# Kernel tuning notes

Hardware: AMD Instinct MI355X
Metric: run time of the kernel (lower is better)

Reference implementation:

```python
import jax, jax.numpy as jnp
import numpy as np

NUM_HEADS = 16
HIDDEN = 1024
HEAD_DIM = HIDDEN // NUM_HEADS


def setup_inputs() -> dict:
    key = jax.random.key(0)
    ks = jax.random.split(key, 9)
    B, S, D = 2, 2048, HIDDEN
    s = 1.0 / np.sqrt(D)
    return {
        "x": jax.random.normal(ks[0], (B, S, D), dtype=jnp.float32),
        "Wq": jax.random.normal(ks[1], (D, D), dtype=jnp.float32) * s,
        "bq": jnp.zeros((D,), dtype=jnp.float32),
        "Wk": jax.random.normal(ks[2], (D, D), dtype=jnp.float32) * s,
        "bk": jnp.zeros((D,), dtype=jnp.float32),
        "Wv": jax.random.normal(ks[3], (D, D), dtype=jnp.float32) * s,
        "bv": jnp.zeros((D,), dtype=jnp.float32),
        "Wo": jax.random.normal(ks[4], (D, D), dtype=jnp.float32) * s,
        "bo": jnp.zeros((D,), dtype=jnp.float32),
    }


def reference(x, Wq, bq, Wk, bk, Wv, bv, Wo, bo):
    B, S, D = x.shape
    H, Hd = NUM_HEADS, HEAD_DIM
    # projections -> [B, H, S, Hd]
    def proj(W, b):
        return (x @ W + b).reshape(B, S, H, Hd).transpose(0, 2, 1, 3)
    q = proj(Wq, bq)
    k = proj(Wk, bk)
    v = proj(Wv, bv)
    scores = jnp.einsum('bhqd,bhkd->bhqk', q, k) / jnp.sqrt(jnp.float32(Hd))
    p_attn = jax.nn.softmax(scores, axis=-1)  # dropout = identity (eval)
    ctx = jnp.einsum('bhqk,bhkd->bhqd', p_attn, v)
    attn_mean = jnp.mean(p_attn, axis=1)  # [B, S, S]
    out = ctx.transpose(0, 2, 1, 3).reshape(B, S, D) @ Wo + bo
    return out, attn_mean
```

## Files before the change

kernel.cpp:

```cpp
#include <hip/hip_runtime.h>
#include <math.h>

#define NUM_HEADS 16
#define HEAD_DIM  64
#define HIDDEN    1024
#define BATCH     2
#define SEQ       2048

#define QSCALE 0.1803368801111204f

typedef short bf16x8 __attribute__((ext_vector_type(8)));
typedef short short4v __attribute__((ext_vector_type(4)));
typedef float f32x4 __attribute__((ext_vector_type(4)));

#if __has_builtin(__builtin_amdgcn_exp2f)
#define EXP2F __builtin_amdgcn_exp2f
#else
#define EXP2F exp2f
#endif

__device__ __forceinline__ short f2bf(float f) {
    union { float f; unsigned int u; } x; x.f = f;
    unsigned int r = x.u + 0x7fffu + ((x.u >> 16) & 1u);
    return (short)(r >> 16);
}

__device__ __forceinline__ unsigned int pack_bf16_trunc(float lo, float hi) {
    return __builtin_amdgcn_perm(__float_as_uint(hi), __float_as_uint(lo), 0x07060302u);
}

__device__ __forceinline__ void async16(const void* g, void* l) {
    __builtin_amdgcn_global_load_lds(
        (const __attribute__((address_space(1))) void*)g,
        (__attribute__((address_space(3))) void*)l, 16, 0, 0);
}

__global__ __launch_bounds__(256)
void convert_x_kernel(const float* __restrict__ x, short* __restrict__ xb)
{
    size_t i = ((size_t)blockIdx.x * 256 + threadIdx.x) * 4;
    float4 v = *(const float4*)&x[i];
    short4v o;
    o.x = f2bf(v.x); o.y = f2bf(v.y); o.z = f2bf(v.z); o.w = f2bf(v.w);
    *(short4v*)&xb[i] = o;
}

__global__ __launch_bounds__(256)
void transpose_w_kernel(const float* __restrict__ Wq, const float* __restrict__ Wk,
                        const float* __restrict__ Wv, const float* __restrict__ Wo,
                        short* __restrict__ Wt4)
{
    __shared__ float t[64][65];
    const int tid = threadIdx.x;
    const int z = blockIdx.z;
    const float* W = (z == 0) ? Wq : (z == 1) ? Wk : (z == 2) ? Wv : Wo;
    short* dst = Wt4 + (size_t)z * HIDDEN * HIDDEN;
    const int c0 = blockIdx.x * 64;
    const int r0 = blockIdx.y * 64;
    const int cl = tid & 63, rw = tid >> 6;
    #pragma unroll
    for (int p = 0; p < 16; ++p) {
        int row = p * 4 + rw;
        t[row][cl] = W[(size_t)(r0 + row) * HIDDEN + c0 + cl];
    }
    __syncthreads();
    #pragma unroll
    for (int p = 0; p < 16; ++p) {
        int orow = p * 4 + rw;
        dst[(size_t)(c0 + orow) * HIDDEN + r0 + cl] = f2bf(t[cl][orow]);
    }
}

__global__ __launch_bounds__(256)
void qkv_proj_kernel(const short* __restrict__ xb, const short* __restrict__ Wt4,
                     const float* __restrict__ bq, const float* __restrict__ bk,
                     const float* __restrict__ bv,
                     short* __restrict__ Qb, short* __restrict__ Kb,
                     short* __restrict__ Vt)
{
    __shared__ short ldsA[128 * 32];
    __shared__ short ldsB[128 * 32];
    const int tid = threadIdx.x;
    const int lane = tid & 63, w = tid >> 6;
    const int l = lane & 15, q = lane >> 4;
    const int n0 = blockIdx.x * 128;
    const int m0 = blockIdx.y * 128;
    const int z  = blockIdx.z;
    const short* Wt = Wt4 + (size_t)z * HIDDEN * HIDDEN;
    const int wm = (w >> 1) * 64, wn = (w & 1) * 64;
    const int kc = q ^ ((l >> 1) & 3);

    f32x4 acc[4][4];
    #pragma unroll
    for (int i = 0; i < 4; ++i)
        #pragma unroll
        for (int j = 0; j < 4; ++j)
            acc[i][j] = (f32x4){0.f, 0.f, 0.f, 0.f};

    for (int k0 = 0; k0 < HIDDEN; k0 += 32) {
        #pragma unroll
        for (int half = 0; half < 2; ++half) {
            int c = half * 256 + tid;
            int row = c >> 2;
            int kcg = (c & 3) ^ ((row >> 1) & 3);
            async16(xb + (size_t)(m0 + row) * HIDDEN + k0 + kcg * 8, &ldsA[c * 8]);
            async16(Wt + (size_t)(n0 + row) * HIDDEN + k0 + kcg * 8, &ldsB[c * 8]);
        }
        __syncthreads();
        bf16x8 af[4], bfr[4];
        #pragma unroll
        for (int i = 0; i < 4; ++i)
            af[i] = *(const bf16x8*)&ldsA[((wm + 16 * i + l) * 4 + kc) * 8];
        #pragma unroll
        for (int j = 0; j < 4; ++j)
            bfr[j] = *(const bf16x8*)&ldsB[((wn + 16 * j + l) * 4 + kc) * 8];
        #pragma unroll
        for (int i = 0; i < 4; ++i)
            #pragma unroll
            for (int j = 0; j < 4; ++j)
                acc[i][j] = __builtin_amdgcn_mfma_f32_16x16x32_bf16(
                    af[i], bfr[j], acc[i][j], 0, 0, 0);
        __syncthreads();
    }

    const float* bias = (z == 0) ? bq : (z == 1) ? bk : bv;
    const float sc = (z == 0) ? QSCALE : 1.0f;
    if (z < 2) {
        short* Ob = (z == 0) ? Qb : Kb;
        #pragma unroll
        for (int j = 0; j < 4; ++j) {
            int n = n0 + wn + 16 * j + l;
            float bval = bias[n];
            int h = n >> 6, hd = n & 63;
            #pragma unroll
            for (int i = 0; i < 4; ++i) {
                #pragma unroll
                for (int reg = 0; reg < 4; ++reg) {
                    int m = m0 + wm + 16 * i + 4 * q + reg;
                    int b_ = m >> 11, s = m & 2047;
                    Ob[(((size_t)(b_ * NUM_HEADS + h) * SEQ) + s) * HEAD_DIM + hd] =
                        f2bf((acc[i][j][reg] + bval) * sc);
                }
            }
        }
    } else {
        #pragma unroll
        for (int j = 0; j < 4; ++j) {
            int n = n0 + wn + 16 * j + l;
            float bval = bias[n];
            int h = n >> 6, hd = n & 63;
            #pragma unroll
            for (int i = 0; i < 4; ++i) {
                int mb = m0 + wm + 16 * i + 4 * q;
                int b_ = mb >> 11, s = mb & 2047;
                short4v pk;
                #pragma unroll
                for (int reg = 0; reg < 4; ++reg)
                    pk[reg] = f2bf(acc[i][j][reg] + bval);
                *(short4v*)&Vt[(((size_t)(b_ * NUM_HEADS + h) * HEAD_DIM) + hd) * SEQ + s] = pk;
            }
        }
    }
}

__global__ __launch_bounds__(256)
void out_proj_kernel(const short* __restrict__ Cb, const short* __restrict__ Wot,
                     const float* __restrict__ bo, float* __restrict__ out)
{
    __shared__ short ldsA[128 * 32];
    __shared__ short ldsB[128 * 32];
    const int tid = threadIdx.x;
    const int lane = tid & 63, w = tid >> 6;
    const int l = lane & 15, q = lane >> 4;
    const int n0 = blockIdx.x * 128;
    const int m0 = blockIdx.y * 128;
    const int wm = (w >> 1) * 64, wn = (w & 1) * 64;
    const int kc = q ^ ((l >> 1) & 3);

    f32x4 acc[4][4];
    #pragma unroll
    for (int i = 0; i < 4; ++i)
        #pragma unroll
        for (int j = 0; j < 4; ++j)
            acc[i][j] = (f32x4){0.f, 0.f, 0.f, 0.f};

    for (int k0 = 0; k0 < HIDDEN; k0 += 32) {
        const int h = k0 >> 6, hdb = k0 & 63;
        #pragma unroll
        for (int half = 0; half < 2; ++half) {
            int c = half * 256 + tid;
            int row = c >> 2;
            int kcg = (c & 3) ^ ((row >> 1) & 3);
            int m = m0 + row;
            int b_ = m >> 11, s = m & 2047;
            async16(Cb + (((size_t)(b_ * NUM_HEADS + h) * SEQ) + s) * HEAD_DIM + hdb + kcg * 8,
                    &ldsA[c * 8]);
            async16(Wot + (size_t)(n0 + row) * HIDDEN + k0 + kcg * 8, &ldsB[c * 8]);
        }
        __syncthreads();
        bf16x8 af[4], bfr[4];
        #pragma unroll
        for (int i = 0; i < 4; ++i)
            af[i] = *(const bf16x8*)&ldsA[((wm + 16 * i + l) * 4 + kc) * 8];
        #pragma unroll
        for (int j = 0; j < 4; ++j)
            bfr[j] = *(const bf16x8*)&ldsB[((wn + 16 * j + l) * 4 + kc) * 8];
        #pragma unroll
        for (int i = 0; i < 4; ++i)
            #pragma unroll
            for (int j = 0; j < 4; ++j)
                acc[i][j] = __builtin_amdgcn_mfma_f32_16x16x32_bf16(
                    af[i], bfr[j], acc[i][j], 0, 0, 0);
        __syncthreads();
    }

    #pragma unroll
    for (int j = 0; j < 4; ++j) {
        int n = n0 + wn + 16 * j + l;
        float bval = bo[n];
        #pragma unroll
        for (int i = 0; i < 4; ++i)
            #pragma unroll
            for (int reg = 0; reg < 4; ++reg) {
                int m = m0 + wm + 16 * i + 4 * q + reg;
                out[(size_t)m * HIDDEN + n] = acc[i][j][reg] + bval;
            }
    }
}

__global__ __launch_bounds__(256)
void flash_kernel(const short* __restrict__ Qb, const short* __restrict__ Kb,
                  const short* __restrict__ Vt, short* __restrict__ Cb,
                  float* __restrict__ Lb)
{
    __shared__ short Qs[128 * 64];
    __shared__ short Ks[64 * 64];
    __shared__ short Vs[64 * 64];
    __shared__ short Ps[4 * 2 * 16 * 72];

    const int tid = threadIdx.x, lane = tid & 63, w = tid >> 6;
    const int l = lane & 15, q = lane >> 4;
    const int q0 = blockIdx.x * 128;
    const int h = blockIdx.y, b = blockIdx.z;
    const size_t base  = (size_t)(b * NUM_HEADS + h) * SEQ * HEAD_DIM;
    const size_t vbase = (size_t)(b * NUM_HEADS + h) * HEAD_DIM * SEQ;
    short* Pw = &Ps[w * 2304];

    #pragma unroll
    for (int i = 0; i < 4; ++i) {
        int c = 256 * i + tid;
        int row = c >> 3;
        int g = ((c & 7) ^ (row & 7)) * 8;
        async16(Qb + base + (size_t)(q0 + row) * HEAD_DIM + g, &Qs[c * 8]);
    }

    const int c1 = tid, c2 = 256 + tid;
    const int row1 = c1 >> 3, row2 = c2 >> 3;
    const int g1 = ((c1 & 7) ^ (row1 & 7)) * 8;
    const int g2 = ((c2 & 7) ^ (row2 & 7)) * 8;
    const short* kp1 = Kb + base + (size_t)row1 * HEAD_DIM + g1;
    const short* kp2 = Kb + base + (size_t)row2 * HEAD_DIM + g2;
    const short* vp1 = Vt + vbase + (size_t)row1 * SEQ + g1;
    const short* vp2 = Vt + vbase + (size_t)row2 * SEQ + g2;

    f32x4 ctx[2][4];
    #pragma unroll
    for (int u = 0; u < 2; ++u)
        #pragma unroll
        for (int t = 0; t < 4; ++t) ctx[u][t] = (f32x4){0.f, 0.f, 0.f, 0.f};
    float l_part[2] = {0.f, 0.f};

    for (int kt = 0; kt < SEQ; kt += 64) {
        async16(kp1, &Ks[c1 * 8]);
        async16(kp2, &Ks[c2 * 8]);
        async16(vp1, &Vs[c1 * 8]);
        async16(vp2, &Vs[c2 * 8]);
        kp1 += 64 * HEAD_DIM; kp2 += 64 * HEAD_DIM;
        vp1 += 64;            vp2 += 64;
        __syncthreads();

        f32x4 st[2][4];
        #pragma unroll
        for (int u = 0; u < 2; ++u)
            #pragma unroll
            for (int t = 0; t < 4; ++t) st[u][t] = (f32x4){0.f, 0.f, 0.f, 0.f};
        #pragma unroll
        for (int ks = 0; ks < 2; ++ks) {
            int cc = (4 * ks + q) ^ (l & 7);
            bf16x8 bq0 = *(const bf16x8*)&Qs[((32 * w + l) * 8 + cc) * 8];
            bf16x8 bq1 = *(const bf16x8*)&Qs[((32 * w + 16 + l) * 8 + cc) * 8];
            #pragma unroll
            for (int t = 0; t < 4; ++t) {
                bf16x8 ak = *(const bf16x8*)&Ks[((16 * t + l) * 8 + cc) * 8];
                st[0][t] = __builtin_amdgcn_mfma_f32_16x16x32_bf16(ak, bq0, st[0][t], 0, 0, 0);
                st[1][t] = __builtin_amdgcn_mfma_f32_16x16x32_bf16(ak, bq1, st[1][t], 0, 0, 0);
            }
        }

        #pragma unroll
        for (int u = 0; u < 2; ++u) {
            #pragma unroll
            for (int t = 0; t < 4; ++t) {
                float p0 = EXP2F(st[u][t][0]);
                float p1 = EXP2F(st[u][t][1]);
                float p2 = EXP2F(st[u][t][2]);
                float p3 = EXP2F(st[u][t][3]);
                l_part[u] += (p0 + p1) + (p2 + p3);
                uint2 pk;
                pk.x = pack_bf16_trunc(p0, p1);
                pk.y = pack_bf16_trunc(p2, p3);
                *(uint2*)&Pw[u * 1152 + l * 72 + 16 * t + 4 * q] = pk;
            }
        }

        #pragma unroll
        for (int ks = 0; ks < 2; ++ks) {
            int cc = (4 * ks + q) ^ (l & 7);
            bf16x8 bp0 = *(const bf16x8*)&Pw[l * 72 + ks * 32 + q * 8];
            bf16x8 bp1 = *(const bf16x8*)&Pw[1152 + l * 72 + ks * 32 + q * 8];
            #pragma unroll
            for (int t = 0; t < 4; ++t) {
                bf16x8 av = *(const bf16x8*)&Vs[((16 * t + l) * 8 + cc) * 8];
                ctx[0][t] = __builtin_amdgcn_mfma_f32_16x16x32_bf16(av, bp0, ctx[0][t], 0, 0, 0);
                ctx[1][t] = __builtin_amdgcn_mfma_f32_16x16x32_bf16(av, bp1, ctx[1][t], 0, 0, 0);
            }
        }
        __syncthreads();
    }

    #pragma unroll
    for (int u = 0; u < 2; ++u) {
        float rs = l_part[u];
        rs += __shfl_xor(rs, 16);
        rs += __shfl_xor(rs, 32);
        float inv_l = 1.0f / rs;
        int s = q0 + 32 * w + 16 * u + l;
        #pragma unroll
        for (int t = 0; t < 4; ++t) {
            short4v pk;
            #pragma unroll
            for (int reg = 0; reg < 4; ++reg)
                pk[reg] = f2bf(ctx[u][t][reg] * inv_l);
            *(short4v*)&Cb[(((size_t)(b * NUM_HEADS + h) * SEQ) + s) * HEAD_DIM + 16 * t + 4 * q] = pk;
        }
        if (q == 0)
            Lb[(size_t)(b * NUM_HEADS + h) * SEQ + s] = rs;
    }
}

__global__ __launch_bounds__(256)
void attn_mean_kernel(const short* __restrict__ Qb, const short* __restrict__ Kb,
                      const float* __restrict__ Lb, float* __restrict__ amean)
{
    __shared__ short Qs[2][64 * 64];
    __shared__ short Ks[2][64 * 64];
    __shared__ float Le[2][64];
    const int tid = threadIdx.x, lane = tid & 63, w = tid >> 6;
    const int l = lane & 15, q = lane >> 4;
    const int k0 = blockIdx.x * 64;
    const int q0 = blockIdx.y * 64;
    const int b  = blockIdx.z;

    f32x4 acc[4];
    #pragma unroll
    for (int t = 0; t < 4; ++t) acc[t] = (f32x4){0.f, 0.f, 0.f, 0.f};

    for (int hp = 0; hp < NUM_HEADS; hp += 2) {
        #pragma unroll
        for (int e = 0; e < 2; ++e) {
            const size_t base = (size_t)(b * NUM_HEADS + hp + e) * SEQ * HEAD_DIM;
            #pragma unroll
            for (int half = 0; half < 2; ++half) {
                int c = half * 256 + tid;
                int row = c >> 3;
                int g = ((c & 7) ^ (row & 7)) * 8;
                async16(Qb + base + (size_t)(q0 + row) * HEAD_DIM + g, &Qs[e][c * 8]);
                async16(Kb + base + (size_t)(k0 + row) * HEAD_DIM + g, &Ks[e][c * 8]);
            }
        }
        if (tid < 128) {
            int e = tid >> 6, r = tid & 63;
            Le[e][r] = 1.0f / Lb[(size_t)(b * NUM_HEADS + hp + e) * SEQ + q0 + r];
        }
        __syncthreads();

        #pragma unroll
        for (int e = 0; e < 2; ++e) {
            bf16x8 ak[2];
            #pragma unroll
            for (int ks = 0; ks < 2; ++ks) {
                int cc = (4 * ks + q) ^ (l & 7);
                ak[ks] = *(const bf16x8*)&Ks[e][((16 * w + l) * 8 + cc) * 8];
            }
            #pragma unroll
            for (int tq = 0; tq < 4; ++tq) {
                f32x4 st = (f32x4){0.f, 0.f, 0.f, 0.f};
                #pragma unroll
                for (int ks = 0; ks < 2; ++ks) {
                    int cc = (4 * ks + q) ^ (l & 7);
                    bf16x8 bqf = *(const bf16x8*)&Qs[e][((16 * tq + l) * 8 + cc) * 8];
                    st = __builtin_amdgcn_mfma_f32_16x16x32_bf16(ak[ks], bqf, st, 0, 0, 0);
                }
                float li = Le[e][16 * tq + l];
                #pragma unroll
                for (int reg = 0; reg < 4; ++reg)
                    acc[tq][reg] += EXP2F(st[reg]) * li;
            }
        }
        __syncthreads();
    }

    const float inv_h = 1.0f / (float)NUM_HEADS;
    #pragma unroll
    for (int tq = 0; tq < 4; ++tq) {
        int row_q = q0 + 16 * tq + l;
        int col_k = k0 + 16 * w + 4 * q;
        f32x4 o;
        #pragma unroll
        for (int reg = 0; reg < 4; ++reg) o[reg] = acc[tq][reg] * inv_h;
        *(f32x4*)&amean[((size_t)b * SEQ + row_q) * SEQ + col_k] = o;
    }
}

extern "C" void kernel_launch(void* const* d_in, const int* in_sizes, int n_in,
                              void* d_out, int out_size, void* d_ws, size_t ws_size,
                              hipStream_t stream)
{
    const float* x  = (const float*)d_in[0];
    const float* Wq = (const float*)d_in[1];
    const float* bq = (const float*)d_in[2];
    const float* Wk = (const float*)d_in[3];
    const float* bk = (const float*)d_in[4];
    const float* Wv = (const float*)d_in[5];
    const float* bv = (const float*)d_in[6];
    const float* Wo = (const float*)d_in[7];
    const float* bo = (const float*)d_in[8];

    float* out   = (float*)d_out;
    float* amean = out + (size_t)BATCH * SEQ * HIDDEN;

    const size_t NELEM = (size_t)BATCH * NUM_HEADS * SEQ * HEAD_DIM;
    short* ws  = (short*)d_ws;
    short* xb  = ws;
    short* Wt4 = xb + NELEM;
    short* Qb  = Wt4 + 4 * (size_t)HIDDEN * HIDDEN;
    short* Kb  = Qb + NELEM;
    short* Vt  = Kb + NELEM;
    short* Cb  = Vt + NELEM;
    float* Lb  = (float*)(Cb + NELEM);

    dim3 blk(256);
    convert_x_kernel<<<dim3(4096), blk, 0, stream>>>(x, xb);
    transpose_w_kernel<<<dim3(16, 16, 4), blk, 0, stream>>>(Wq, Wk, Wv, Wo, Wt4);
    qkv_proj_kernel<<<dim3(8, 32, 3), blk, 0, stream>>>(xb, Wt4, bq, bk, bv, Qb, Kb, Vt);
    flash_kernel<<<dim3(SEQ / 128, NUM_HEADS, BATCH), blk, 0, stream>>>(Qb, Kb, Vt, Cb, Lb);
    attn_mean_kernel<<<dim3(SEQ / 64, SEQ / 64, BATCH), blk, 0, stream>>>(Qb, Kb, Lb, amean);
    out_proj_kernel<<<dim3(8, 32), blk, 0, stream>>>(Cb, Wt4 + 3 * (size_t)HIDDEN * HIDDEN, bo, out);
}
```

Before: 267.5 us.

## Enlarge attn-mean key tile, shrink out-proj tile, merge prep kernels

The attention-mean kernel now has each block cover 256 keys instead of 64 and process one head per iteration. Q fragments are loaded once per head and reused across four key sub-tiles per wave, which cuts redundant Q loads and the block count. The output projection moves to 64-row M tiles so more blocks run on the 256 CUs. The x conversion and weight transpose are merged into a single launch. The larger attention-mean tile raises register and LDS use, which may lower occupancy.

```diff
diff --git a/kernel.cpp b/kernel.cpp
--- a/kernel.cpp
+++ b/kernel.cpp
@@ -36,27 +36,29 @@
 }
 
 __global__ __launch_bounds__(256)
-void convert_x_kernel(const float* __restrict__ x, short* __restrict__ xb)
-{
-    size_t i = ((size_t)blockIdx.x * 256 + threadIdx.x) * 4;
-    float4 v = *(const float4*)&x[i];
-    short4v o;
-    o.x = f2bf(v.x); o.y = f2bf(v.y); o.z = f2bf(v.z); o.w = f2bf(v.w);
-    *(short4v*)&xb[i] = o;
-}
-
-__global__ __launch_bounds__(256)
-void transpose_w_kernel(const float* __restrict__ Wq, const float* __restrict__ Wk,
-                        const float* __restrict__ Wv, const float* __restrict__ Wo,
-                        short* __restrict__ Wt4)
+void prep_kernel(const float* __restrict__ x,
+                 const float* __restrict__ Wq, const float* __restrict__ Wk,
+                 const float* __restrict__ Wv, const float* __restrict__ Wo,
+                 short* __restrict__ xb, short* __restrict__ Wt4)
 {
     __shared__ float t[64][65];
     const int tid = threadIdx.x;
-    const int z = blockIdx.z;
+    const int bid = blockIdx.x;
+    if (bid < 4096) {
+        size_t i = ((size_t)bid * 256 + tid) * 4;
+        float4 v = *(const float4*)&x[i];
+        short4v o;
+        o.x = f2bf(v.x); o.y = f2bf(v.y); o.z = f2bf(v.z); o.w = f2bf(v.w);
+        *(short4v*)&xb[i] = o;
+        return;
+    }
+    const int tb = bid - 4096;
+    const int z  = tb >> 8;
+    const int cx = tb & 15, cy = (tb >> 4) & 15;
     const float* W = (z == 0) ? Wq : (z == 1) ? Wk : (z == 2) ? Wv : Wo;
     short* dst = Wt4 + (size_t)z * HIDDEN * HIDDEN;
-    const int c0 = blockIdx.x * 64;
-    const int r0 = blockIdx.y * 64;
+    const int c0 = cx * 64;
+    const int r0 = cy * 64;
     const int cl = tid & 63, rw = tid >> 6;
     #pragma unroll
     for (int p = 0; p < 16; ++p) {
@@ -167,62 +169,66 @@
 void out_proj_kernel(const short* __restrict__ Cb, const short* __restrict__ Wot,
                      const float* __restrict__ bo, float* __restrict__ out)
 {
-    __shared__ short ldsA[128 * 32];
+    __shared__ short ldsA[64 * 32];
     __shared__ short ldsB[128 * 32];
     const int tid = threadIdx.x;
     const int lane = tid & 63, w = tid >> 6;
     const int l = lane & 15, q = lane >> 4;
     const int n0 = blockIdx.x * 128;
-    const int m0 = blockIdx.y * 128;
-    const int wm = (w >> 1) * 64, wn = (w & 1) * 64;
+    const int m0 = blockIdx.y * 64;
     const int kc = q ^ ((l >> 1) & 3);
 
-    f32x4 acc[4][4];
+    f32x4 acc[4][2];
     #pragma unroll
     for (int i = 0; i < 4; ++i)
         #pragma unroll
-        for (int j = 0; j < 4; ++j)
+        for (int j = 0; j < 2; ++j)
             acc[i][j] = (f32x4){0.f, 0.f, 0.f, 0.f};
 
     for (int k0 = 0; k0 < HIDDEN; k0 += 32) {
         const int h = k0 >> 6, hdb = k0 & 63;
-        #pragma unroll
-        for (int half = 0; half < 2; ++half) {
-            int c = half * 256 + tid;
+        {
+            int c = tid;
             int row = c >> 2;
             int kcg = (c & 3) ^ ((row >> 1) & 3);
             int m = m0 + row;
             int b_ = m >> 11, s = m & 2047;
             async16(Cb + (((size_t)(b_ * NUM_HEADS + h) * SEQ) + s) * HEAD_DIM + hdb + kcg * 8,
                     &ldsA[c * 8]);
+        }
+        #pragma unroll
+        for (int half = 0; half < 2; ++half) {
+            int c = half * 256 + tid;
+            int row = c >> 2;
+            int kcg = (c & 3) ^ ((row >> 1) & 3);
             async16(Wot + (size_t)(n0 + row) * HIDDEN + k0 + kcg * 8, &ldsB[c * 8]);
         }
         __syncthreads();
-        bf16x8 af[4], bfr[4];
+        bf16x8 af[4], bfr[2];
         #pragma unroll
         for (int i = 0; i < 4; ++i)
-            af[i] = *(const bf16x8*)&ldsA[((wm + 16 * i + l) * 4 + kc) * 8];
-        #pragma unroll
-        for (int j = 0; j < 4; ++j)
-            bfr[j] = *(const bf16x8*)&ldsB[((wn + 16 * j + l) * 4 + kc) * 8];
+            af[i] = *(const bf16x8*)&ldsA[((16 * i + l) * 4 + kc) * 8];
+        #pragma unroll
+        for (int j = 0; j < 2; ++j)
+            bfr[j] = *(const bf16x8*)&ldsB[((32 * w + 16 * j + l) * 4 + kc) * 8];
         #pragma unroll
         for (int i = 0; i < 4; ++i)
             #pragma unroll
-            for (int j = 0; j < 4; ++j)
+            for (int j = 0; j < 2; ++j)
                 acc[i][j] = __builtin_amdgcn_mfma_f32_16x16x32_bf16(
                     af[i], bfr[j], acc[i][j], 0, 0, 0);
         __syncthreads();
     }
 
     #pragma unroll
-    for (int j = 0; j < 4; ++j) {
-        int n = n0 + wn + 16 * j + l;
+    for (int j = 0; j < 2; ++j) {
+        int n = n0 + 32 * w + 16 * j + l;
         float bval = bo[n];
         #pragma unroll
         for (int i = 0; i < 4; ++i)
             #pragma unroll
             for (int reg = 0; reg < 4; ++reg) {
-                int m = m0 + wm + 16 * i + 4 * q + reg;
+                int m = m0 + 16 * i + 4 * q + reg;
                 out[(size_t)m * HIDDEN + n] = acc[i][j][reg] + bval;
             }
     }
@@ -352,59 +358,78 @@
 void attn_mean_kernel(const short* __restrict__ Qb, const short* __restrict__ Kb,
                       const float* __restrict__ Lb, float* __restrict__ amean)
 {
-    __shared__ short Qs[2][64 * 64];
-    __shared__ short Ks[2][64 * 64];
-    __shared__ float Le[2][64];
+    __shared__ short Qs[64 * 64];
+    __shared__ short Ks[256 * 64];
+    __shared__ float Le[64];
     const int tid = threadIdx.x, lane = tid & 63, w = tid >> 6;
     const int l = lane & 15, q = lane >> 4;
-    const int k0 = blockIdx.x * 64;
+    const int k0 = blockIdx.x * 256;
     const int q0 = blockIdx.y * 64;
     const int b  = blockIdx.z;
-
-    f32x4 acc[4];
-    #pragma unroll
-    for (int t = 0; t < 4; ++t) acc[t] = (f32x4){0.f, 0.f, 0.f, 0.f};
-
-    for (int hp = 0; hp < NUM_HEADS; hp += 2) {
-        #pragma unroll
-        for (int e = 0; e < 2; ++e) {
-            const size_t base = (size_t)(b * NUM_HEADS + hp + e) * SEQ * HEAD_DIM;
-            #pragma unroll
-            for (int half = 0; half < 2; ++half) {
-                int c = half * 256 + tid;
-                int row = c >> 3;
-                int g = ((c & 7) ^ (row & 7)) * 8;
-                async16(Qb + base + (size_t)(q0 + row) * HEAD_DIM + g, &Qs[e][c * 8]);
-                async16(Kb + base + (size_t)(k0 + row) * HEAD_DIM + g, &Ks[e][c * 8]);
-            }
-        }
-        if (tid < 128) {
-            int e = tid >> 6, r = tid & 63;
-            Le[e][r] = 1.0f / Lb[(size_t)(b * NUM_HEADS + hp + e) * SEQ + q0 + r];
-        }
-        __syncthreads();
-
-        #pragma unroll
-        for (int e = 0; e < 2; ++e) {
-            bf16x8 ak[2];
+    const size_t HSTRIDE = (size_t)SEQ * HEAD_DIM;
+
+    const short* qp[2];
+    const short* kp[8];
+    {
+        const size_t base0 = (size_t)(b * NUM_HEADS) * HSTRIDE;
+        #pragma unroll
+        for (int i = 0; i < 2; ++i) {
+            int c = 256 * i + tid;
+            int row = c >> 3;
+            int g = ((c & 7) ^ (row & 7)) * 8;
+            qp[i] = Qb + base0 + (size_t)(q0 + row) * HEAD_DIM + g;
+        }
+        #pragma unroll
+        for (int i = 0; i < 8; ++i) {
+            int c = 256 * i + tid;
+            int row = c >> 3;
+            int g = ((c & 7) ^ (row & 7)) * 8;
+            kp[i] = Kb + base0 + (size_t)(k0 + row) * HEAD_DIM + g;
+        }
+    }
+
+    f32x4 macc[4][4];
+    #pragma unroll
+    for (int tk = 0; tk < 4; ++tk)
+        #pragma unroll
+        for (int tq = 0; tq < 4; ++tq)
+            macc[tk][tq] = (f32x4){0.f, 0.f, 0.f, 0.f};
+
+    for (int h = 0; h < NUM_HEADS; ++h) {
+        #pragma unroll
+        for (int i = 0; i < 2; ++i) { async16(qp[i], &Qs[(256 * i + tid) * 8]); qp[i] += HSTRIDE; }
+        #pragma unroll
+        for (int i = 0; i < 8; ++i) { async16(kp[i], &Ks[(256 * i + tid) * 8]); kp[i] += HSTRIDE; }
+        if (tid < 64)
+            Le[tid] = 1.0f / Lb[(size_t)(b * NUM_HEADS + h) * SEQ + q0 + tid];
+        __syncthreads();
+
+        bf16x8 bq[4][2];
+        #pragma unroll
+        for (int tq = 0; tq < 4; ++tq)
             #pragma unroll
             for (int ks = 0; ks < 2; ++ks) {
                 int cc = (4 * ks + q) ^ (l & 7);
-                ak[ks] = *(const bf16x8*)&Ks[e][((16 * w + l) * 8 + cc) * 8];
+                bq[tq][ks] = *(const bf16x8*)&Qs[((16 * tq + l) * 8 + cc) * 8];
+            }
+
+        #pragma unroll
+        for (int tk = 0; tk < 4; ++tk) {
+            bf16x8 ak[2];
+            #pragma unroll
+            for (int ks = 0; ks < 2; ++ks) {
+                int cc = (4 * ks + q) ^ (l & 7);
+                ak[ks] = *(const bf16x8*)&Ks[((64 * w + 16 * tk + l) * 8 + cc) * 8];
             }
             #pragma unroll
             for (int tq = 0; tq < 4; ++tq) {
                 f32x4 st = (f32x4){0.f, 0.f, 0.f, 0.f};
-                #pragma unroll
-                for (int ks = 0; ks < 2; ++ks) {
-                    int cc = (4 * ks + q) ^ (l & 7);
-                    bf16x8 bqf = *(const bf16x8*)&Qs[e][((16 * tq + l) * 8 + cc) * 8];
-                    st = __builtin_amdgcn_mfma_f32_16x16x32_bf16(ak[ks], bqf, st, 0, 0, 0);
-                }
-                float li = Le[e][16 * tq + l];
+                st = __builtin_amdgcn_mfma_f32_16x16x32_bf16(ak[0], bq[tq][0], st, 0, 0, 0);
+                st = __builtin_amdgcn_mfma_f32_16x16x32_bf16(ak[1], bq[tq][1], st, 0, 0, 0);
+                float li = Le[16 * tq + l];
                 #pragma unroll
                 for (int reg = 0; reg < 4; ++reg)
-                    acc[tq][reg] += EXP2F(st[reg]) * li;
+                    macc[tk][tq][reg] += EXP2F(st[reg]) * li;
             }
         }
         __syncthreads();
@@ -414,11 +439,14 @@
     #pragma unroll
     for (int tq = 0; tq < 4; ++tq) {
         int row_q = q0 + 16 * tq + l;
-        int col_k = k0 + 16 * w + 4 * q;
-        f32x4 o;
-        #pragma unroll
-        for (int reg = 0; reg < 4; ++reg) o[reg] = acc[tq][reg] * inv_h;
-        *(f32x4*)&amean[((size_t)b * SEQ + row_q) * SEQ + col_k] = o;
+        #pragma unroll
+        for (int tk = 0; tk < 4; ++tk) {
+            int col_k = k0 + 64 * w + 16 * tk + 4 * q;
+            f32x4 o;
+            #pragma unroll
+            for (int reg = 0; reg < 4; ++reg) o[reg] = macc[tk][tq][reg] * inv_h;
+            *(f32x4*)&amean[((size_t)b * SEQ + row_q) * SEQ + col_k] = o;
+        }
     }
 }
 
@@ -450,10 +478,9 @@
     float* Lb  = (float*)(Cb + NELEM);
 
     dim3 blk(256);
-    convert_x_kernel<<<dim3(4096), blk, 0, stream>>>(x, xb);
-    transpose_w_kernel<<<dim3(16, 16, 4), blk, 0, stream>>>(Wq, Wk, Wv, Wo, Wt4);
+    prep_kernel<<<dim3(4096 + 1024), blk, 0, stream>>>(x, Wq, Wk, Wv, Wo, xb, Wt4);
     qkv_proj_kernel<<<dim3(8, 32, 3), blk, 0, stream>>>(xb, Wt4, bq, bk, bv, Qb, Kb, Vt);
     flash_kernel<<<dim3(SEQ / 128, NUM_HEADS, BATCH), blk, 0, stream>>>(Qb, Kb, Vt, Cb, Lb);
-    attn_mean_kernel<<<dim3(SEQ / 64, SEQ / 64, BATCH), blk, 0, stream>>>(Qb, Kb, Lb, amean);
-    out_proj_kernel<<<dim3(8, 32), blk, 0, stream>>>(Cb, Wt4 + 3 * (size_t)HIDDEN * HIDDEN, bo, out);
-}
+    attn_mean_kernel<<<dim3(SEQ / 256, SEQ / 64, BATCH), blk, 0, stream>>>(Qb, Kb, Lb, amean);
+    out_proj_kernel<<<dim3(8, 64), blk, 0, stream>>>(Cb, Wt4 + 3 * (size_t)HIDDEN * HIDDEN, bo, out);
+}
```

New measurement: 262.2 us. -2.0%, faster.
